# Performance work log

Hardware: AMD Instinct MI355X
Metric: run time of the kernel (lower is better)

## Reference

```python
import jax, jax.numpy as jnp
import numpy as np
import math

EMBED_DIMS = 256
NUM_LANDMARKS = 40  # hard-coded k=40 in the original module
B, N = 2, 8192


def setup_inputs() -> dict:
    key = jax.random.key(0)
    ks = jax.random.split(key, 9)
    C = EMBED_DIMS
    w = lambda k: jax.random.normal(k, (C, C), dtype=jnp.float32) * 0.02
    b = lambda k: jax.random.normal(k, (C,), dtype=jnp.float32) * 0.02
    return {
        "query": jax.random.normal(ks[0], (B, N, C), dtype=jnp.float32),
        "Wq": w(ks[1]), "bq": b(ks[2]),
        "Wk": w(ks[3]), "bk": b(ks[4]),
        "Wv": w(ks[5]), "bv": b(ks[6]),
        "Wo": w(ks[7]), "bo": b(ks[8]),
    }


def reference(query, Wq, bq, Wk, bk, Wv, bv, Wo, bo):
    # key = value = identity = query (defaults in the original forward)
    C = query.shape[-1]
    scaling = math.sqrt(C)

    q = query @ Wq.T + bq  # [B, N, C]
    k = query @ Wk.T + bk
    v = query @ Wv.T + bv

    # Full similarity only to score keys: score_m[b, m] = sum_n sim_nm[b, n, m]
    sim_nm = jnp.einsum('bnc,bmc->bnm', q, k) / scaling  # [B, N, N]
    score_m = sim_nm.sum(axis=1)                          # [B, N]

    _, top_idx = jax.lax.top_k(score_m, NUM_LANDMARKS)    # [B, 40]
    selected = jnp.take_along_axis(k, top_idx[:, :, None], axis=1)  # [B, 40, C]

    sim_qn = jax.nn.softmax(jnp.einsum('bnc,bkc->bnk', q, selected) / scaling, axis=-1)  # [B, N, 40]
    sim_km = jax.nn.softmax(jnp.einsum('bmc,bkc->bmk', k, selected) / scaling, axis=-1)  # [B, N, 40]

    sim_qk = jnp.einsum('bnk,bmk->bnm', sim_qn, sim_km)   # [B, N, N]
    out = jnp.einsum('bnm,bmc->bnc', sim_qk, v)           # [B, N, C]
    out = out @ Wo.T + bo
    return query + out  # identity residual; dropouts are identity at p=0
```

## Files before the change

kernel.cpp:

```cpp
#include <hip/hip_runtime.h>
#include <cstddef>
#include <cstdint>

#define BATCH 2
#define SEQ 8192
#define CH 256
#define NLM 40
#define NLMP 48
#define MROWS (BATCH * SEQ)
#define INV_SCALE 0.0625f
#define NCBLK 256

typedef unsigned short ushort_t;
typedef __attribute__((ext_vector_type(8))) short short8;
typedef __attribute__((ext_vector_type(4))) float floatx4;

__device__ __forceinline__ ushort_t f2bf(float f) {
    unsigned int u = __float_as_uint(f);
    u += 0x7FFFu + ((u >> 16) & 1u);
    return (ushort_t)(u >> 16);
}
__device__ __forceinline__ float bf2f(ushort_t u) {
    return __uint_as_float(((unsigned)u) << 16);
}

__device__ __forceinline__ void gload_lds16(const ushort_t* g, ushort_t* l) {
    __builtin_amdgcn_global_load_lds(
        (const __attribute__((address_space(1))) unsigned int*)g,
        (__attribute__((address_space(3))) unsigned int*)l, 16, 0, 0);
}

__global__ __launch_bounds__(256) void convert_colsum(const float* __restrict__ x,
                                                      ushort_t* __restrict__ xbf,
                                                      float* __restrict__ partial) {
    __shared__ float red[4][256];
    const int b = blockIdx.y;
    const int r0 = blockIdx.x * 32;
    const int t = threadIdx.x;
    const int c4 = (t & 63) * 4;
    const int rg = t >> 6;
    const float* base = x + ((size_t)b * SEQ + r0) * 256;
    ushort_t* obase = xbf + ((size_t)b * SEQ + r0) * 256;
    float4 s = {0.f, 0.f, 0.f, 0.f};
#pragma unroll
    for (int i = 0; i < 8; i++) {
        const int r = rg + i * 4;
        const float4 a = *(const float4*)&base[(size_t)r * 256 + c4];
        uint2 o;
        o.x = f2bf(a.x) | ((unsigned)f2bf(a.y) << 16);
        o.y = f2bf(a.z) | ((unsigned)f2bf(a.w) << 16);
        *(uint2*)&obase[(size_t)r * 256 + c4] = o;
        s.x += a.x; s.y += a.y; s.z += a.z; s.w += a.w;
    }
    *(float4*)&red[rg][c4] = s;
    __syncthreads();
    const float tot = red[0][t] + red[1][t] + red[2][t] + red[3][t];
    partial[((size_t)b * NCBLK + blockIdx.x) * 256 + t] = tot;
}

__global__ __launch_bounds__(1024) void ws_kernel(const float* __restrict__ partial,
                                                  const float* __restrict__ Wq,
                                                  const float* __restrict__ bq,
                                                  const float* __restrict__ Wk,
                                                  float* __restrict__ ws,
                                                  float* __restrict__ tmat) {
    const int b = blockIdx.x;
    __shared__ float xs[256];
    __shared__ float qs[256];
    __shared__ float ppart[4][256];
    const int t = threadIdx.x;
    {
        float* tz = tmat + (size_t)b * NLM * 256;
        for (int i = t; i < NLM * 256; i += 1024) tz[i] = 0.f;
    }
    {
        const int c = t & 255, qd = t >> 8;
        const float* pb = partial + ((size_t)b * NCBLK + qd * 64) * 256 + c;
        float a = 0.f;
#pragma unroll 8
        for (int i = 0; i < 64; i++) a += pb[(size_t)i * 256];
        ppart[qd][c] = a;
    }
    __syncthreads();
    if (t < 256) xs[t] = ppart[0][t] + ppart[1][t] + ppart[2][t] + ppart[3][t];
    __syncthreads();
    const int lane = t & 63, w = t >> 6;
    for (int g = 0; g < 16; g++) {
        const int o = w * 16 + g;
        const float4 wq = *(const float4*)&Wq[(size_t)o * 256 + lane * 4];
        const float4 x4 = *(const float4*)&xs[lane * 4];
        float d = wq.x * x4.x + wq.y * x4.y + wq.z * x4.z + wq.w * x4.w;
#pragma unroll
        for (int off = 32; off >= 1; off >>= 1) d += __shfl_down(d, off);
        if (lane == 0) qs[o] = d + 8192.0f * bq[o];
    }
    __syncthreads();
    const int c = t & 255, part = t >> 8;
    float a = 0.f;
    for (int o = part * 64; o < part * 64 + 64; o++)
        a += Wk[(size_t)o * 256 + c] * qs[o];
    ppart[part][c] = a;
    __syncthreads();
    if (t < 256)
        ws[b * 256 + t] = ppart[0][t] + ppart[1][t] + ppart[2][t] + ppart[3][t];
}

__global__ __launch_bounds__(256) void gemm_qkv_score(const ushort_t* __restrict__ xbf,
                                                      const float* __restrict__ Wq,
                                                      const float* __restrict__ Wk,
                                                      const float* __restrict__ Wv,
                                                      const float* __restrict__ bq,
                                                      const float* __restrict__ bk,
                                                      const float* __restrict__ bv,
                                                      ushort_t* __restrict__ qkv,
                                                      const float* __restrict__ query,
                                                      const float* __restrict__ ws,
                                                      float* __restrict__ score) {
    __shared__ __align__(16) char smem[24576];
    ushort_t* As = (ushort_t*)smem;
    ushort_t* Bs = (ushort_t*)(smem + 16384);
    ushort_t* Es = (ushort_t*)smem;
    const int z = blockIdx.z;
    const int t = threadIdx.x;
    const int lane = t & 63;
    const int w = t >> 6;

    if (z == 3) {
        const int blk = blockIdx.y * 4 + blockIdx.x;
#pragma unroll
        for (int i = 0; i < 8; i++) {
            const int g = blk * 32 + i * 4 + w;
            const int b = g >> 13;
            const int m = g & 8191;
            const float4 kv = *(const float4*)&query[(size_t)g * 256 + lane * 4];
            const float4 qs = *(const float4*)&ws[b * 256 + lane * 4];
            float d = kv.x * qs.x + kv.y * qs.y + kv.z * qs.z + kv.w * qs.w;
#pragma unroll
            for (int off = 32; off >= 1; off >>= 1) d += __shfl_down(d, off);
            if (lane == 0) score[(size_t)b * SEQ + m] = d * INV_SCALE;
        }
        return;
    }

    const float* __restrict__ W = (z == 0) ? Wq : (z == 1) ? Wk : Wv;
    const float* __restrict__ bias = (z == 0) ? bq : (z == 1) ? bk : bv;
    ushort_t* __restrict__ out = qkv + (size_t)z * MROWS * 256;
    const int o0 = blockIdx.x * 64;
    const int m0 = blockIdx.y * 128;
    const int quad = lane >> 4;
    const int l16 = lane & 15;
    const int xsw = l16 & 7;

    floatx4 acc[2][4];
#pragma unroll
    for (int rt = 0; rt < 2; rt++)
#pragma unroll
        for (int ct = 0; ct < 4; ct++) acc[rt][ct] = (floatx4){0.f, 0.f, 0.f, 0.f};

    for (int kc = 0; kc < 256; kc += 64) {
#pragma unroll
        for (int q = 0; q < 4; q++) {
            const int r0 = w * 32 + q * 8;
            gload_lds16(&xbf[(size_t)(m0 + r0 + (lane >> 3)) * 256 + kc +
                             (((lane & 7) ^ (lane >> 3)) * 8)],
                        &As[r0 * 64]);
        }
#pragma unroll
        for (int u = 0; u < 2; u++) {
            const int cid = t + u * 256;
            const int row = cid >> 3;
            const int cch = cid & 7;
            const float* wp = &W[(size_t)(o0 + row) * 256 + kc + cch * 8];
            const float4 a = *(const float4*)wp;
            const float4 c = *(const float4*)(wp + 4);
            uint4 o;
            o.x = f2bf(a.x) | ((unsigned)f2bf(a.y) << 16);
            o.y = f2bf(a.z) | ((unsigned)f2bf(a.w) << 16);
            o.z = f2bf(c.x) | ((unsigned)f2bf(c.y) << 16);
            o.w = f2bf(c.z) | ((unsigned)f2bf(c.w) << 16);
            *(uint4*)&Bs[row * 64 + ((cch ^ (row & 7)) * 8)] = o;
        }
        __syncthreads();
#pragma unroll
        for (int s = 0; s < 2; s++) {
            short8 a[2], bf[4];
#pragma unroll
            for (int rt = 0; rt < 2; rt++)
                a[rt] = *(const short8*)&As[(w * 32 + rt * 16 + l16) * 64 +
                                            (((s * 4 + quad) ^ xsw) * 8)];
#pragma unroll
            for (int ct = 0; ct < 4; ct++)
                bf[ct] = *(const short8*)&Bs[(ct * 16 + l16) * 64 +
                                             (((s * 4 + quad) ^ xsw) * 8)];
#pragma unroll
            for (int rt = 0; rt < 2; rt++)
#pragma unroll
                for (int ct = 0; ct < 4; ct++)
                    acc[rt][ct] = __builtin_amdgcn_mfma_f32_16x16x32_bf16(
                        a[rt], bf[ct], acc[rt][ct], 0, 0, 0);
        }
        __syncthreads();
    }

#pragma unroll
    for (int rt = 0; rt < 2; rt++) {
#pragma unroll
        for (int ct = 0; ct < 4; ct++) {
            const int col = ct * 16 + l16;
            const float bb = bias[o0 + col];
#pragma unroll
            for (int reg = 0; reg < 4; reg++) {
                const int row = w * 32 + rt * 16 + quad * 4 + reg;
                Es[row * 72 + col] = f2bf(acc[rt][ct][reg] + bb);
            }
        }
    }
    __syncthreads();
#pragma unroll
    for (int u = 0; u < 4; u++) {
        const int cid = t + u * 256;
        const int row = cid >> 3;
        const int off = (cid & 7) * 8;
        *(uint4*)&out[(size_t)(m0 + row) * 256 + o0 + off] =
            *(const uint4*)&Es[row * 72 + off];
    }
}

__global__ __launch_bounds__(1024) void topk_gather(const float* __restrict__ score,
                                                    const ushort_t* __restrict__ kmat,
                                                    ushort_t* __restrict__ sel) {
    const int b = blockIdx.x;
    const int t = threadIdx.x;
    __shared__ unsigned hist[256];
    __shared__ unsigned wsum[64];
    __shared__ unsigned sPrefix, sMask, sRem, sNeq;
    __shared__ int sNgt;
    __shared__ int top[NLM];
    __shared__ unsigned topkey[NLM];

    unsigned key[8];
#pragma unroll
    for (int j = 0; j < 8; j++) {
        const unsigned u = __float_as_uint(score[(size_t)b * SEQ + t + j * 1024]);
        key[j] = u ^ (unsigned)(((int)u >> 31) | 0x80000000);
    }
    if (t == 0) { sPrefix = 0; sMask = 0; sRem = NLM; sNgt = 0; sNeq = 0; }

    for (int lvl = 0; lvl < 4; lvl++) {
        const int shift = 24 - 8 * lvl;
        if (t < 256) hist[t] = 0;
        __syncthreads();
        const unsigned pfx = sPrefix, msk = sMask;
#pragma unroll
        for (int j = 0; j < 8; j++)
            if (((key[j] ^ pfx) & msk) == 0)
                atomicAdd(&hist[(key[j] >> shift) & 255u], 1u);
        __syncthreads();
        if (t < 64) wsum[t] = hist[t * 4] + hist[t * 4 + 1] + hist[t * 4 + 2] + hist[t * 4 + 3];
        __syncthreads();
        if (t == 0) {
            unsigned rem = sRem, cum = 0;
            int g = 63;
            for (; g > 0; g--) { if (cum + wsum[g] >= rem) break; cum += wsum[g]; }
            int d = g * 4 + 3;
            for (; d > g * 4; d--) { if (cum + hist[d] >= rem) break; cum += hist[d]; }
            sRem = rem - cum;
            sPrefix |= ((unsigned)d) << shift;
            sMask |= 255u << shift;
        }
        __syncthreads();
    }
    const unsigned K40 = sPrefix;
    const unsigned rem = sRem;
    const int ngt = NLM - (int)rem;

#pragma unroll
    for (int j = 0; j < 8; j++) {
        if (key[j] > K40) {
            const int slot = atomicAdd(&sNgt, 1);
            top[slot] = t + j * 1024; topkey[slot] = key[j];
        } else if (key[j] == K40) {
            const unsigned e = atomicAdd(&sNeq, 1u);
            if (e < rem) {
                const int slot = ngt + (int)e;
                top[slot] = t + j * 1024; topkey[slot] = key[j];
            }
        }
    }
    __syncthreads();

    if (t < 64) {
        unsigned long long c = (t < NLM)
            ? ((((unsigned long long)(~topkey[t])) << 32) | (unsigned)top[t])
            : 0xFFFFFFFFFFFFFFFFull;
#pragma unroll
        for (int kk = 2; kk <= 64; kk <<= 1) {
#pragma unroll
            for (int j = kk >> 1; j >= 1; j >>= 1) {
                const unsigned long long o = __shfl_xor(c, j);
                const bool takeMin = ((t & kk) == 0) == ((t & j) == 0);
                const bool less = c < o;
                c = (takeMin == less) ? c : o;
            }
        }
        if (t < NLM) top[t] = (int)(c & 0xFFFFFFFFu);
    }
    __syncthreads();

    for (int f = t; f < NLMP * 256; f += 1024) {
        const int j = f >> 8;
        const int cc = f & 255;
        sel[(size_t)b * NLMP * 256 + f] =
            (j < NLM) ? kmat[((size_t)b * SEQ + top[j]) * 256 + cc] : (ushort_t)0;
    }
}

__global__ __launch_bounds__(256, 4) void sim_fused(const ushort_t* __restrict__ qbf,
                                                    const ushort_t* __restrict__ kbf,
                                                    const ushort_t* __restrict__ vbf,
                                                    const ushort_t* __restrict__ sel,
                                                    float* __restrict__ simq,
                                                    float* __restrict__ tmat) {
    __shared__ __align__(16) char smem[43008];
    float (*Ps)[40]  = (float(*)[40])smem;
    ushort_t* Vs     = (ushort_t*)(smem + 10240);
    const int b = blockIdx.y;
    const int n0 = blockIdx.x * 64;
    const int t = threadIdx.x;
    const int lane = t & 63;
    const int w = t >> 6;
    const int quad = lane >> 4;
    const int l16 = lane & 15;
    const ushort_t* __restrict__ A = (blockIdx.z == 0) ? qbf : kbf;
    const ushort_t* __restrict__ Arow = A + ((size_t)b * SEQ + n0 + w * 16 + l16) * 256;
    const ushort_t* __restrict__ Sb = sel + (size_t)b * NLMP * 256 + (size_t)l16 * 256;

    floatx4 acc[3];
#pragma unroll
    for (int ct = 0; ct < 3; ct++) acc[ct] = (floatx4){0.f, 0.f, 0.f, 0.f};

#pragma unroll
    for (int ks = 0; ks < 8; ks++) {
        const int ko = ks * 32 + quad * 8;
        const short8 a  = *(const short8*)&Arow[ko];
        const short8 b0 = *(const short8*)&Sb[ko];
        const short8 b1 = *(const short8*)&Sb[16 * 256 + ko];
        const short8 b2 = *(const short8*)&Sb[32 * 256 + ko];
        acc[0] = __builtin_amdgcn_mfma_f32_16x16x32_bf16(a, b0, acc[0], 0, 0, 0);
        acc[1] = __builtin_amdgcn_mfma_f32_16x16x32_bf16(a, b1, acc[1], 0, 0, 0);
        acc[2] = __builtin_amdgcn_mfma_f32_16x16x32_bf16(a, b2, acc[2], 0, 0, 0);
    }

    const bool v2ok = (l16 < 8);
    float p0[4], p1[4], p2[4];
#pragma unroll
    for (int reg = 0; reg < 4; reg++) {
        const float l0 = acc[0][reg] * INV_SCALE;
        const float l1 = acc[1][reg] * INV_SCALE;
        const float l2 = acc[2][reg] * INV_SCALE;
        float m = fmaxf(l0, l1);
        if (v2ok) m = fmaxf(m, l2);
        m = fmaxf(m, __shfl_xor(m, 1));
        m = fmaxf(m, __shfl_xor(m, 2));
        m = fmaxf(m, __shfl_xor(m, 4));
        m = fmaxf(m, __shfl_xor(m, 8));
        const float e0 = expf(l0 - m);
        const float e1 = expf(l1 - m);
        const float e2 = v2ok ? expf(l2 - m) : 0.f;
        float s = e0 + e1 + e2;
        s += __shfl_xor(s, 1);
        s += __shfl_xor(s, 2);
        s += __shfl_xor(s, 4);
        s += __shfl_xor(s, 8);
        const float inv = 1.f / s;
        p0[reg] = e0 * inv; p1[reg] = e1 * inv; p2[reg] = e2 * inv;
    }

    const int row0 = w * 16 + quad * 4;
    if (blockIdx.z == 0) {
        float* __restrict__ dst = &simq[((size_t)b * SEQ + n0 + row0) * NLM];
#pragma unroll
        for (int reg = 0; reg < 4; reg++) {
            float* __restrict__ d2 = dst + reg * NLM;
            d2[l16] = p0[reg];
            d2[16 + l16] = p1[reg];
            if (v2ok) d2[32 + l16] = p2[reg];
        }
        return;
    }

#pragma unroll
    for (int reg = 0; reg < 4; reg++) {
        Ps[row0 + reg][l16] = p0[reg];
        Ps[row0 + reg][16 + l16] = p1[reg];
        if (v2ok) Ps[row0 + reg][32 + l16] = p2[reg];
    }
#pragma unroll
    for (int u = 0; u < 8; u++) {
        gload_lds16(&vbf[((size_t)b * SEQ + n0 + w * 2 + u * 8 + (lane >> 5)) * 256 +
                         (lane & 31) * 8],
                    &Vs[(w * 2 + u * 8) * 256]);
    }
    __syncthreads();

    float tac[40];
#pragma unroll
    for (int j = 0; j < 40; j++) tac[j] = 0.f;

#pragma unroll 2
    for (int m = 0; m < 64; m++) {
        const float vv = bf2f(Vs[m * 256 + t]);
#pragma unroll
        for (int j4 = 0; j4 < 10; j4++) {
            const float4 p = *(const float4*)&Ps[m][j4 * 4];
            tac[j4 * 4 + 0] = fmaf(p.x, vv, tac[j4 * 4 + 0]);
            tac[j4 * 4 + 1] = fmaf(p.y, vv, tac[j4 * 4 + 1]);
            tac[j4 * 4 + 2] = fmaf(p.z, vv, tac[j4 * 4 + 2]);
            tac[j4 * 4 + 3] = fmaf(p.w, vv, tac[j4 * 4 + 3]);
        }
    }
#pragma unroll
    for (int j = 0; j < 40; j++)
        atomicAdd(&tmat[(size_t)b * NLM * 256 + j * 256 + t], tac[j]);
}

__global__ __launch_bounds__(256) void out_pre_kernel(const float* __restrict__ simq,
                                                      const float* __restrict__ tmat,
                                                      ushort_t* __restrict__ outp_bf) {
    __shared__ float Pm[64][40];
    const int g0 = blockIdx.x * 64;
    const int b = g0 >> 13;
    const int t = threadIdx.x;
    float* pflat = &Pm[0][0];
    for (int f = t; f < 64 * NLM; f += 256) pflat[f] = simq[(size_t)g0 * NLM + f];
    float tc[40];
#pragma unroll
    for (int l = 0; l < 40; l++) tc[l] = tmat[(size_t)b * NLM * 256 + l * 256 + t];
    __syncthreads();
#pragma unroll 2
    for (int m = 0; m < 64; m++) {
        float a = 0.f;
#pragma unroll
        for (int j4 = 0; j4 < 10; j4++) {
            const float4 p = *(const float4*)&Pm[m][j4 * 4];
            a = fmaf(p.x, tc[j4 * 4 + 0], a);
            a = fmaf(p.y, tc[j4 * 4 + 1], a);
            a = fmaf(p.z, tc[j4 * 4 + 2], a);
            a = fmaf(p.w, tc[j4 * 4 + 3], a);
        }
        outp_bf[((size_t)g0 + m) * 256 + t] = f2bf(a);
    }
}

__global__ __launch_bounds__(256) void gemm_out(const ushort_t* __restrict__ Abf,
                                                const float* __restrict__ Wo,
                                                const float* __restrict__ bias,
                                                const float* __restrict__ resid,
                                                float* __restrict__ out) {
    __shared__ __align__(16) char smem[34816];
    ushort_t* As = (ushort_t*)smem;
    ushort_t* Bs = (ushort_t*)(smem + 16384);
    float* Ft = (float*)smem;
    const int t = threadIdx.x;
    const int o0 = blockIdx.x * 64;
    const int m0 = blockIdx.y * 128;
    const int lane = t & 63;
    const int w = t >> 6;
    const int quad = lane >> 4;
    const int l16 = lane & 15;
    const int xsw = l16 & 7;

    floatx4 acc[2][4];
#pragma unroll
    for (int rt = 0; rt < 2; rt++)
#pragma unroll
        for (int ct = 0; ct < 4; ct++) acc[rt][ct] = (floatx4){0.f, 0.f, 0.f, 0.f};

    for (int kc = 0; kc < 256; kc += 64) {
#pragma unroll
        for (int q = 0; q < 4; q++) {
            const int r0 = w * 32 + q * 8;
            gload_lds16(&Abf[(size_t)(m0 + r0 + (lane >> 3)) * 256 + kc +
                             (((lane & 7) ^ (lane >> 3)) * 8)],
                        &As[r0 * 64]);
        }
#pragma unroll
        for (int u = 0; u < 2; u++) {
            const int cid = t + u * 256;
            const int row = cid >> 3;
            const int cch = cid & 7;
            const float* wp = &Wo[(size_t)(o0 + row) * 256 + kc + cch * 8];
            const float4 a = *(const float4*)wp;
            const float4 c = *(const float4*)(wp + 4);
            uint4 o;
            o.x = f2bf(a.x) | ((unsigned)f2bf(a.y) << 16);
            o.y = f2bf(a.z) | ((unsigned)f2bf(a.w) << 16);
            o.z = f2bf(c.x) | ((unsigned)f2bf(c.y) << 16);
            o.w = f2bf(c.z) | ((unsigned)f2bf(c.w) << 16);
            *(uint4*)&Bs[row * 64 + ((cch ^ (row & 7)) * 8)] = o;
        }
        __syncthreads();
#pragma unroll
        for (int s = 0; s < 2; s++) {
            short8 a[2], bf[4];
#pragma unroll
            for (int rt = 0; rt < 2; rt++)
                a[rt] = *(const short8*)&As[(w * 32 + rt * 16 + l16) * 64 +
                                            (((s * 4 + quad) ^ xsw) * 8)];
#pragma unroll
            for (int ct = 0; ct < 4; ct++)
                bf[ct] = *(const short8*)&Bs[(ct * 16 + l16) * 64 +
                                             (((s * 4 + quad) ^ xsw) * 8)];
#pragma unroll
            for (int rt = 0; rt < 2; rt++)
#pragma unroll
                for (int ct = 0; ct < 4; ct++)
                    acc[rt][ct] = __builtin_amdgcn_mfma_f32_16x16x32_bf16(
                        a[rt], bf[ct], acc[rt][ct], 0, 0, 0);
        }
        __syncthreads();
    }

#pragma unroll
    for (int rt = 0; rt < 2; rt++) {
#pragma unroll
        for (int ct = 0; ct < 4; ct++) {
            const int col = ct * 16 + l16;
            const float bb = bias[o0 + col];
#pragma unroll
            for (int reg = 0; reg < 4; reg++) {
                const int row = w * 32 + rt * 16 + quad * 4 + reg;
                Ft[row * 68 + col] = acc[rt][ct][reg] + bb;
            }
        }
    }
    __syncthreads();
#pragma unroll
    for (int u = 0; u < 8; u++) {
        const int cid = t + u * 256;
        const int row = cid >> 4;
        const int off = (cid & 15) * 4;
        const float4 v = *(const float4*)&Ft[row * 68 + off];
        const float4 r4 = *(const float4*)&resid[(size_t)(m0 + row) * 256 + o0 + off];
        float4 o;
        o.x = v.x + r4.x; o.y = v.y + r4.y; o.z = v.z + r4.z; o.w = v.w + r4.w;
        *(float4*)&out[(size_t)(m0 + row) * 256 + o0 + off] = o;
    }
}

extern "C" void kernel_launch(void* const* d_in, const int* in_sizes, int n_in,
                              void* d_out, int out_size, void* d_ws, size_t ws_size,
                              hipStream_t stream) {
    const float* query = (const float*)d_in[0];
    const float* Wq = (const float*)d_in[1];
    const float* bq = (const float*)d_in[2];
    const float* Wk = (const float*)d_in[3];
    const float* bk = (const float*)d_in[4];
    const float* Wv = (const float*)d_in[5];
    const float* bv = (const float*)d_in[6];
    const float* Wo = (const float*)d_in[7];
    const float* bo = (const float*)d_in[8];
    float* out = (float*)d_out;

    char* p = (char*)d_ws;
    float* simq  = (float*)p;            p += (size_t)MROWS * NLM * 4;
    ushort_t* selbf = (ushort_t*)p;      p += (size_t)BATCH * NLMP * 256 * 2;
    float* tmat  = (float*)p;            p += (size_t)BATCH * NLM * 256 * 4;
    float* partial = (float*)p;          p += (size_t)BATCH * NCBLK * 256 * 4;
    float* ws    = (float*)p;            p += (size_t)BATCH * 256 * 4;
    float* score = (float*)p;            p += (size_t)BATCH * SEQ * 4;
    ushort_t* qkv = (ushort_t*)p;        p += (size_t)3 * MROWS * 256 * 2;
    ushort_t* xbf = (ushort_t*)p;        p += (size_t)MROWS * 256 * 2;
    ushort_t* qbf = qkv;
    ushort_t* kbf = qkv + (size_t)MROWS * 256;
    ushort_t* vbf = qkv + (size_t)2 * MROWS * 256;
    ushort_t* outp_bf = xbf;

    const dim3 blk(256);

    convert_colsum<<<dim3(SEQ / 32, BATCH), blk, 0, stream>>>(query, xbf, partial);
    ws_kernel<<<dim3(BATCH), dim3(1024), 0, stream>>>(partial, Wq, bq, Wk, ws, tmat);

    gemm_qkv_score<<<dim3(4, MROWS / 128, 4), blk, 0, stream>>>(
        xbf, Wq, Wk, Wv, bq, bk, bv, qkv, query, ws, score);

    topk_gather<<<dim3(BATCH), dim3(1024), 0, stream>>>(score, kbf, selbf);

    sim_fused<<<dim3(SEQ / 64, BATCH, 2), blk, 0, stream>>>(qbf, kbf, vbf, selbf, simq, tmat);

    out_pre_kernel<<<dim3(MROWS / 64), blk, 0, stream>>>(simq, tmat, outp_bf);
    gemm_out<<<dim3(4, MROWS / 128), blk, 0, stream>>>(outp_bf, Wo, bo, query, out);
}
```

Before: 191.9 us.

## Process four key tiles per block in sim_fused to cut tmat atomics

The key-side branch of sim_fused now loops over four 64-row chunks per block and keeps the 40x256 T accumulator in registers across them. This makes each block issue its atomicAdds to tmat once per 256 rows instead of once per 64, a quarter of the global atomic traffic. Blocks with blockIdx.x >= 32 on that side now exit immediately, so the work sits in fewer, longer-running blocks, with an added barrier between chunks. A separate small change in the reduction kernel preloads the 16 Wq rows into registers and unrolls the Wk loop.

```diff
diff --git a/kernel.cpp b/kernel.cpp
--- a/kernel.cpp
+++ b/kernel.cpp
@@ -85,18 +85,25 @@
     if (t < 256) xs[t] = ppart[0][t] + ppart[1][t] + ppart[2][t] + ppart[3][t];
     __syncthreads();
     const int lane = t & 63, w = t >> 6;
-    for (int g = 0; g < 16; g++) {
-        const int o = w * 16 + g;
-        const float4 wq = *(const float4*)&Wq[(size_t)o * 256 + lane * 4];
+    {
+        float4 wq[16];
+#pragma unroll
+        for (int g = 0; g < 16; g++)
+            wq[g] = *(const float4*)&Wq[(size_t)(w * 16 + g) * 256 + lane * 4];
         const float4 x4 = *(const float4*)&xs[lane * 4];
-        float d = wq.x * x4.x + wq.y * x4.y + wq.z * x4.z + wq.w * x4.w;
-#pragma unroll
-        for (int off = 32; off >= 1; off >>= 1) d += __shfl_down(d, off);
-        if (lane == 0) qs[o] = d + 8192.0f * bq[o];
+#pragma unroll
+        for (int g = 0; g < 16; g++) {
+            const int o = w * 16 + g;
+            float d = wq[g].x * x4.x + wq[g].y * x4.y + wq[g].z * x4.z + wq[g].w * x4.w;
+#pragma unroll
+            for (int off = 32; off >= 1; off >>= 1) d += __shfl_down(d, off);
+            if (lane == 0) qs[o] = d + 8192.0f * bq[o];
+        }
     }
     __syncthreads();
     const int c = t & 255, part = t >> 8;
     float a = 0.f;
+#pragma unroll 16
     for (int o = part * 64; o < part * 64 + 64; o++)
         a += Wk[(size_t)o * 256 + c] * qs[o];
     ppart[part][c] = a;
@@ -325,98 +332,136 @@
     float (*Ps)[40]  = (float(*)[40])smem;
     ushort_t* Vs     = (ushort_t*)(smem + 10240);
     const int b = blockIdx.y;
-    const int n0 = blockIdx.x * 64;
     const int t = threadIdx.x;
     const int lane = t & 63;
     const int w = t >> 6;
     const int quad = lane >> 4;
     const int l16 = lane & 15;
-    const ushort_t* __restrict__ A = (blockIdx.z == 0) ? qbf : kbf;
-    const ushort_t* __restrict__ Arow = A + ((size_t)b * SEQ + n0 + w * 16 + l16) * 256;
+    const bool v2ok = (l16 < 8);
     const ushort_t* __restrict__ Sb = sel + (size_t)b * NLMP * 256 + (size_t)l16 * 256;
-
-    floatx4 acc[3];
-#pragma unroll
-    for (int ct = 0; ct < 3; ct++) acc[ct] = (floatx4){0.f, 0.f, 0.f, 0.f};
-
-#pragma unroll
-    for (int ks = 0; ks < 8; ks++) {
-        const int ko = ks * 32 + quad * 8;
-        const short8 a  = *(const short8*)&Arow[ko];
-        const short8 b0 = *(const short8*)&Sb[ko];
-        const short8 b1 = *(const short8*)&Sb[16 * 256 + ko];
-        const short8 b2 = *(const short8*)&Sb[32 * 256 + ko];
-        acc[0] = __builtin_amdgcn_mfma_f32_16x16x32_bf16(a, b0, acc[0], 0, 0, 0);
-        acc[1] = __builtin_amdgcn_mfma_f32_16x16x32_bf16(a, b1, acc[1], 0, 0, 0);
-        acc[2] = __builtin_amdgcn_mfma_f32_16x16x32_bf16(a, b2, acc[2], 0, 0, 0);
-    }
-
-    const bool v2ok = (l16 < 8);
-    float p0[4], p1[4], p2[4];
-#pragma unroll
-    for (int reg = 0; reg < 4; reg++) {
-        const float l0 = acc[0][reg] * INV_SCALE;
-        const float l1 = acc[1][reg] * INV_SCALE;
-        const float l2 = acc[2][reg] * INV_SCALE;
-        float m = fmaxf(l0, l1);
-        if (v2ok) m = fmaxf(m, l2);
-        m = fmaxf(m, __shfl_xor(m, 1));
-        m = fmaxf(m, __shfl_xor(m, 2));
-        m = fmaxf(m, __shfl_xor(m, 4));
-        m = fmaxf(m, __shfl_xor(m, 8));
-        const float e0 = expf(l0 - m);
-        const float e1 = expf(l1 - m);
-        const float e2 = v2ok ? expf(l2 - m) : 0.f;
-        float s = e0 + e1 + e2;
-        s += __shfl_xor(s, 1);
-        s += __shfl_xor(s, 2);
-        s += __shfl_xor(s, 4);
-        s += __shfl_xor(s, 8);
-        const float inv = 1.f / s;
-        p0[reg] = e0 * inv; p1[reg] = e1 * inv; p2[reg] = e2 * inv;
-    }
-
     const int row0 = w * 16 + quad * 4;
+
     if (blockIdx.z == 0) {
+        const int n0 = blockIdx.x * 64;
+        const ushort_t* __restrict__ Arow =
+            qbf + ((size_t)b * SEQ + n0 + w * 16 + l16) * 256;
+        floatx4 acc[3];
+#pragma unroll
+        for (int ct = 0; ct < 3; ct++) acc[ct] = (floatx4){0.f, 0.f, 0.f, 0.f};
+#pragma unroll
+        for (int ks = 0; ks < 8; ks++) {
+            const int ko = ks * 32 + quad * 8;
+            const short8 a  = *(const short8*)&Arow[ko];
+            const short8 b0 = *(const short8*)&Sb[ko];
+            const short8 b1 = *(const short8*)&Sb[16 * 256 + ko];
+            const short8 b2 = *(const short8*)&Sb[32 * 256 + ko];
+            acc[0] = __builtin_amdgcn_mfma_f32_16x16x32_bf16(a, b0, acc[0], 0, 0, 0);
+            acc[1] = __builtin_amdgcn_mfma_f32_16x16x32_bf16(a, b1, acc[1], 0, 0, 0);
+            acc[2] = __builtin_amdgcn_mfma_f32_16x16x32_bf16(a, b2, acc[2], 0, 0, 0);
+        }
         float* __restrict__ dst = &simq[((size_t)b * SEQ + n0 + row0) * NLM];
 #pragma unroll
         for (int reg = 0; reg < 4; reg++) {
+            const float l0 = acc[0][reg] * INV_SCALE;
+            const float l1 = acc[1][reg] * INV_SCALE;
+            const float l2 = acc[2][reg] * INV_SCALE;
+            float m = fmaxf(l0, l1);
+            if (v2ok) m = fmaxf(m, l2);
+            m = fmaxf(m, __shfl_xor(m, 1));
+            m = fmaxf(m, __shfl_xor(m, 2));
+            m = fmaxf(m, __shfl_xor(m, 4));
+            m = fmaxf(m, __shfl_xor(m, 8));
+            const float e0 = expf(l0 - m);
+            const float e1 = expf(l1 - m);
+            const float e2 = v2ok ? expf(l2 - m) : 0.f;
+            float s = e0 + e1 + e2;
+            s += __shfl_xor(s, 1);
+            s += __shfl_xor(s, 2);
+            s += __shfl_xor(s, 4);
+            s += __shfl_xor(s, 8);
+            const float inv = 1.f / s;
             float* __restrict__ d2 = dst + reg * NLM;
-            d2[l16] = p0[reg];
-            d2[16 + l16] = p1[reg];
-            if (v2ok) d2[32 + l16] = p2[reg];
+            d2[l16] = e0 * inv;
+            d2[16 + l16] = e1 * inv;
+            if (v2ok) d2[32 + l16] = e2 * inv;
         }
         return;
     }
 
-#pragma unroll
-    for (int reg = 0; reg < 4; reg++) {
-        Ps[row0 + reg][l16] = p0[reg];
-        Ps[row0 + reg][16 + l16] = p1[reg];
-        if (v2ok) Ps[row0 + reg][32 + l16] = p2[reg];
-    }
-#pragma unroll
-    for (int u = 0; u < 8; u++) {
-        gload_lds16(&vbf[((size_t)b * SEQ + n0 + w * 2 + u * 8 + (lane >> 5)) * 256 +
-                         (lane & 31) * 8],
-                    &Vs[(w * 2 + u * 8) * 256]);
-    }
-    __syncthreads();
+    if (blockIdx.x >= 32) return;
+    const int nbase = blockIdx.x * 256;
 
     float tac[40];
 #pragma unroll
     for (int j = 0; j < 40; j++) tac[j] = 0.f;
 
+    for (int ck = 0; ck < 4; ck++) {
+        const int n0 = nbase + ck * 64;
+        const ushort_t* __restrict__ Arow =
+            kbf + ((size_t)b * SEQ + n0 + w * 16 + l16) * 256;
+        floatx4 acc[3];
+#pragma unroll
+        for (int ct = 0; ct < 3; ct++) acc[ct] = (floatx4){0.f, 0.f, 0.f, 0.f};
+#pragma unroll
+        for (int ks = 0; ks < 8; ks++) {
+            const int ko = ks * 32 + quad * 8;
+            const short8 a  = *(const short8*)&Arow[ko];
+            const short8 b0 = *(const short8*)&Sb[ko];
+            const short8 b1 = *(const short8*)&Sb[16 * 256 + ko];
+            const short8 b2 = *(const short8*)&Sb[32 * 256 + ko];
+            acc[0] = __builtin_amdgcn_mfma_f32_16x16x32_bf16(a, b0, acc[0], 0, 0, 0);
+            acc[1] = __builtin_amdgcn_mfma_f32_16x16x32_bf16(a, b1, acc[1], 0, 0, 0);
+            acc[2] = __builtin_amdgcn_mfma_f32_16x16x32_bf16(a, b2, acc[2], 0, 0, 0);
+        }
+        float p0[4], p1[4], p2[4];
+#pragma unroll
+        for (int reg = 0; reg < 4; reg++) {
+            const float l0 = acc[0][reg] * INV_SCALE;
+            const float l1 = acc[1][reg] * INV_SCALE;
+            const float l2 = acc[2][reg] * INV_SCALE;
+            float m = fmaxf(l0, l1);
+            if (v2ok) m = fmaxf(m, l2);
+            m = fmaxf(m, __shfl_xor(m, 1));
+            m = fmaxf(m, __shfl_xor(m, 2));
+            m = fmaxf(m, __shfl_xor(m, 4));
+            m = fmaxf(m, __shfl_xor(m, 8));
+            const float e0 = expf(l0 - m);
+            const float e1 = expf(l1 - m);
+            const float e2 = v2ok ? expf(l2 - m) : 0.f;
+            float s = e0 + e1 + e2;
+            s += __shfl_xor(s, 1);
+            s += __shfl_xor(s, 2);
+            s += __shfl_xor(s, 4);
+            s += __shfl_xor(s, 8);
+            const float inv = 1.f / s;
+            p0[reg] = e0 * inv; p1[reg] = e1 * inv; p2[reg] = e2 * inv;
+        }
+        if (ck > 0) __syncthreads();
+#pragma unroll
+        for (int reg = 0; reg < 4; reg++) {
+            Ps[row0 + reg][l16] = p0[reg];
+            Ps[row0 + reg][16 + l16] = p1[reg];
+            if (v2ok) Ps[row0 + reg][32 + l16] = p2[reg];
+        }
+#pragma unroll
+        for (int u = 0; u < 8; u++) {
+            gload_lds16(&vbf[((size_t)b * SEQ + n0 + w * 2 + u * 8 + (lane >> 5)) * 256 +
+                             (lane & 31) * 8],
+                        &Vs[(w * 2 + u * 8) * 256]);
+        }
+        __syncthreads();
+
 #pragma unroll 2
-    for (int m = 0; m < 64; m++) {
-        const float vv = bf2f(Vs[m * 256 + t]);
-#pragma unroll
-        for (int j4 = 0; j4 < 10; j4++) {
-            const float4 p = *(const float4*)&Ps[m][j4 * 4];
-            tac[j4 * 4 + 0] = fmaf(p.x, vv, tac[j4 * 4 + 0]);
-            tac[j4 * 4 + 1] = fmaf(p.y, vv, tac[j4 * 4 + 1]);
-            tac[j4 * 4 + 2] = fmaf(p.z, vv, tac[j4 * 4 + 2]);
-            tac[j4 * 4 + 3] = fmaf(p.w, vv, tac[j4 * 4 + 3]);
+        for (int m = 0; m < 64; m++) {
+            const float vv = bf2f(Vs[m * 256 + t]);
+#pragma unroll
+            for (int j4 = 0; j4 < 10; j4++) {
+                const float4 p = *(const float4*)&Ps[m][j4 * 4];
+                tac[j4 * 4 + 0] = fmaf(p.x, vv, tac[j4 * 4 + 0]);
+                tac[j4 * 4 + 1] = fmaf(p.y, vv, tac[j4 * 4 + 1]);
+                tac[j4 * 4 + 2] = fmaf(p.z, vv, tac[j4 * 4 + 2]);
+                tac[j4 * 4 + 3] = fmaf(p.w, vv, tac[j4 * 4 + 3]);
+            }
         }
     }
 #pragma unroll
```

New measurement: 225.9 us. 17.7% more time.
